# Kernel tuning notes

Hardware: AMD Instinct MI355X
Metric: run time of the kernel (lower is better)

Reference implementation:

```python
import jax, jax.numpy as jnp
import numpy as np

NUM_LAYERS = 4
HIDDEN = 64
IN_CH = 3
OUT_CH = 1


def setup_inputs() -> dict:
    key = jax.random.key(0)
    ks = jax.random.split(key, 16)
    s = 0.1  # weight init scale
    x = jax.random.normal(ks[0], (2, 64, 64, IN_CH), dtype=jnp.float32)
    lift_w = jax.random.normal(ks[1], (IN_CH, HIDDEN), dtype=jnp.float32) * s
    lift_b = jax.random.normal(ks[2], (HIDDEN,), dtype=jnp.float32) * s
    blk_w = jax.random.normal(ks[3], (NUM_LAYERS, HIDDEN, HIDDEN), dtype=jnp.float32) * s
    blk_b = jax.random.normal(ks[4], (NUM_LAYERS, HIDDEN), dtype=jnp.float32) * s
    q_w = jax.random.normal(ks[5], (NUM_LAYERS, HIDDEN, HIDDEN), dtype=jnp.float32) * s
    q_b = jax.random.normal(ks[6], (NUM_LAYERS, HIDDEN), dtype=jnp.float32) * s
    k_w = jax.random.normal(ks[7], (NUM_LAYERS, HIDDEN, HIDDEN), dtype=jnp.float32) * s
    k_b = jax.random.normal(ks[8], (NUM_LAYERS, HIDDEN), dtype=jnp.float32) * s
    v_w = jax.random.normal(ks[9], (NUM_LAYERS, HIDDEN, HIDDEN), dtype=jnp.float32) * s
    v_b = jax.random.normal(ks[10], (NUM_LAYERS, HIDDEN), dtype=jnp.float32) * s
    proj_w = jax.random.normal(ks[11], (HIDDEN, OUT_CH), dtype=jnp.float32) * s
    proj_b = jax.random.normal(ks[12], (OUT_CH,), dtype=jnp.float32) * s
    return {"x": x, "lift_w": lift_w, "lift_b": lift_b,
            "blk_w": blk_w, "blk_b": blk_b,
            "q_w": q_w, "q_b": q_b, "k_w": k_w, "k_b": k_b,
            "v_w": v_w, "v_b": v_b, "proj_w": proj_w, "proj_b": proj_b}


def reference(x, lift_w, lift_b, blk_w, blk_b, q_w, q_b, k_w, k_b, v_w, v_b, proj_w, proj_b):
    prefix = x.shape[:-1]           # (B, H, W)
    B = x.shape[0]
    xf = x.reshape(B, -1, x.shape[-1])   # [B, N, in_ch]
    N = xf.shape[1]
    h = xf @ lift_w + lift_b             # [B, N, d]
    d = h.shape[-1]
    scale = 1.0 / jnp.sqrt(jnp.float32(d))
    for i in range(NUM_LAYERS):
        q = h @ q_w[i] + q_b[i]
        k = h @ k_w[i] + k_b[i]
        v = h @ v_w[i] + v_b[i]
        # full dense kernel, as in torch.bmm(q, k^T)/sqrt(d)
        kern = jnp.einsum('bnd,bmd->bnm', q, k) * scale     # [B, N, N]
        integral = jnp.einsum('bnm,bmd->bnd', kern, v) / N  # [B, N, d]
        wh = h @ blk_w[i] + blk_b[i]
        h = jax.nn.gelu(wh + integral, approximate=False)   # torch F.gelu default = exact erf
    out = h @ proj_w + proj_b                               # [B, N, out_ch]
    return out.reshape(*prefix, out.shape[-1])
```

## Files before the change

### kernel.cpp

```cpp
#include <hip/hip_runtime.h>
#include <hip/hip_bf16.h>
#include <math.h>


#define NLAYER 4
#define NB 2
#define NN 4096
#define DD 64
#define RPB 32
#define NT 256
#define NBLK 256
#define SHP 68
#define C0F (1.0f/32768.0f)
#define PSZ 2304
#define NCH 128
#define CHW 18

typedef __hip_bfloat16 bf16;
typedef unsigned long long u64t;

__device__ __forceinline__ float b2f(const bf16 v) { return __bfloat162float(v); }

template <typename T> struct Acc;
template <> struct Acc<float> {
    static __device__ __forceinline__ float ld(const void* p, int i) { return ((const float*)p)[i]; }
    static __device__ __forceinline__ void st(void* p, int i, float v) { ((float*)p)[i] = v; }
};
template <> struct Acc<bf16> {
    static __device__ __forceinline__ float ld(const void* p, int i) { return b2f(((const bf16*)p)[i]); }
    static __device__ __forceinline__ void st(void* p, int i, float v) { ((bf16*)p)[i] = __float2bfloat16(v); }
};

__device__ __forceinline__ float gelu_exact(float x) {
    return 0.5f * x * (1.0f + erff(x * 0.70710678118654752f));
}

__device__ __forceinline__ float2 ldc2(const float* p) {
    u64t v = __hip_atomic_load((const u64t*)p, __ATOMIC_RELAXED, __HIP_MEMORY_SCOPE_AGENT);
    float2 r;
    r.x = __uint_as_float((unsigned)v);
    r.y = __uint_as_float((unsigned)(v >> 32));
    return r;
}
__device__ __forceinline__ void stc2(float* p, float a, float b) {
    u64t v = ((u64t)__float_as_uint(b) << 32) | (u64t)__float_as_uint(a);
    __hip_atomic_store((u64t*)p, v, __ATOMIC_RELAXED, __HIP_MEMORY_SCOPE_AGENT);
}
__device__ __forceinline__ unsigned ldw(unsigned* p) {
    return __hip_atomic_load(p, __ATOMIC_RELAXED, __HIP_MEMORY_SCOPE_AGENT);
}
__device__ __forceinline__ void stw(unsigned* p, unsigned v) {
    __hip_atomic_store(p, v, __ATOMIC_RELAXED, __HIP_MEMORY_SCOPE_AGENT);
}
__device__ __forceinline__ void pollw(unsigned* p, unsigned ep) {
    int guard = 0;
    while (ldw(p) < ep && ++guard < (1 << 17)) __builtin_amdgcn_s_sleep(8);
}

__device__ __forceinline__ void mm4x4(float (&acc)[4][4],
    float4 L0, float4 L1, float4 L2, float4 L3,
    float4 R0, float4 R1, float4 R2, float4 R3)
{
    const float L[4][4] = {{L0.x,L0.y,L0.z,L0.w},{L1.x,L1.y,L1.z,L1.w},
                           {L2.x,L2.y,L2.z,L2.w},{L3.x,L3.y,L3.z,L3.w}};
    const float R[4][4] = {{R0.x,R0.y,R0.z,R0.w},{R1.x,R1.y,R1.z,R1.w},
                           {R2.x,R2.y,R2.z,R2.w},{R3.x,R3.y,R3.z,R3.w}};
    #pragma unroll
    for (int a = 0; a < 4; a++)
        #pragma unroll
        for (int k = 0; k < 4; k++)
            #pragma unroll
            for (int b = 0; b < 4; b++)
                acc[a][b] += L[a][k] * R[k][b];
}

__device__ __forceinline__ void outer4x4(float (&acc)[4][4], float4 A, float4 B)
{
    const float Aa[4] = {A.x, A.y, A.z, A.w};
    const float Ba[4] = {B.x, B.y, B.z, B.w};
    #pragma unroll
    for (int a = 0; a < 4; a++)
        #pragma unroll
        for (int b = 0; b < 4; b++)
            acc[a][b] += Aa[a] * Ba[b];
}


template <typename T>
__device__ void run_net(
    const void* x, const void* lw, const void* lb,
    const void* blkw, const void* blkb,
    const void* qw, const void* qb, const void* kw, const void* kb,
    const void* vw, const void* vb, const void* pw, const void* pb,
    void* out, float* Gpart, float* Gg,
    unsigned* aflag, unsigned* cflag,
    float* smem, int blk, int t)
{
    float (*sH)[SHP] = (float(*)[SHP])(smem);
    float (*B1)[SHP] = (float(*)[SHP])(smem + 2176);
    float (*B2)[SHP] = (float(*)[SHP])(smem + 6528);
    float (*B3)[SHP] = (float(*)[SHP])(smem + 10880);
    float (*B4)[SHP] = (float(*)[SHP])(smem + 15232);
    float* PS  = smem + 10880;
    float* RED = smem + 10880;
    float* sS  = smem + 19584;
    float* suS = smem + 19648;
    float* bkS = smem + 19712;
    float* bqS = smem + 19776;
    float* bvS = smem + 19840;
    float* beS = smem + 19904;
    float (*red)[DD] = (float(*)[DD])(smem + 19968);

    const int row0 = blk * RPB;
    const int bb = blk >> 7;
    const int r = t >> 4, c4 = (t & 15) << 2;
    const int i4 = t >> 4, j4 = t & 15;
    const int r0 = i4 << 2, c0 = j4 << 2;

    #pragma unroll
    for (int a = 0; a < 2; a++) {
        const int row = r + 16 * a, gr = row0 + row;
        float x0 = Acc<T>::ld(x, gr * 3 + 0);
        float x1 = Acc<T>::ld(x, gr * 3 + 1);
        float x2 = Acc<T>::ld(x, gr * 3 + 2);
        float o[4];
        #pragma unroll
        for (int b = 0; b < 4; b++) {
            int c = c4 + b;
            o[b] = Acc<T>::ld(lb, c) + x0 * Acc<T>::ld(lw, c)
                 + x1 * Acc<T>::ld(lw, DD + c) + x2 * Acc<T>::ld(lw, 2 * DD + c);
        }
        *(float4*)&sH[row][c4] = make_float4(o[0], o[1], o[2], o[3]);
    }
    __syncthreads();

    for (int layer = 0; layer < NLAYER; layer++) {
        const unsigned ep = (unsigned)(layer + 1);
        float* GgL = Gg + (size_t)(layer * NB + bb) * PSZ;
        const int wOff = layer * DD * DD, bOff = layer * DD;

        {
            if (i4 <= j4) {
                float m[4][4];
                #pragma unroll
                for (int a = 0; a < 4; a++)
                    #pragma unroll
                    for (int b = 0; b < 4; b++) m[a][b] = 0.f;
                #pragma unroll 8
                for (int n = 0; n < RPB; n++)
                    outer4x4(m, *(const float4*)&sH[n][r0], *(const float4*)&sH[n][c0]);
                float* dst = PS + (i4 * (33 - i4) / 2 + (j4 - i4)) * 16;
                #pragma unroll
                for (int a = 0; a < 4; a++)
                    #pragma unroll
                    for (int b = 0; b < 4; b++) dst[a * 4 + b] = m[a][b];
            }
            if (t < DD) {
                float ss = 0.f;
                #pragma unroll 8
                for (int n = 0; n < RPB; n++) ss += sH[n][t];
                PS[2176 + t] = ss;
                PS[2240 + t] = 0.f;
            }
        }
        __syncthreads();
        {
            float* slot = Gpart + (size_t)blk * PSZ;
            #pragma unroll
            for (int k2 = 0; k2 < 4; k2++) {
                const int idx = 2 * (t + k2 * NT);
                stc2(&slot[idx], PS[idx], PS[idx + 1]);
            }
            if (t < 128) {
                const int idx = 2 * (t + 4 * NT);
                stc2(&slot[idx], PS[idx], PS[idx + 1]);
            }
        }
        __syncthreads();
        if (t == 0) stw(&aflag[blk], ep);

        for (int i2 = t; i2 < DD * DD; i2 += NT) {
            B2[i2 >> 6][i2 & 63] = Acc<T>::ld(vw, wOff + i2);
            B4[i2 >> 6][i2 & 63] = Acc<T>::ld(kw, wOff + i2);
        }
        if (t < DD) {
            bkS[t] = Acc<T>::ld(kb, bOff + t);
            bqS[t] = Acc<T>::ld(qb, bOff + t);
            bvS[t] = Acc<T>::ld(vb, bOff + t);
        }

        {
            if (t < NCH) pollw(&aflag[bb * NCH + t], ep);
            __syncthreads();
            const int chunk = blk & (NCH - 1);
            if (t < 144) {
                const int g = t / 9, p2 = t % 9;
                const float* base = Gpart + (size_t)(bb * NCH + g * 8) * PSZ
                                  + chunk * CHW + 2 * p2;
                float ax = 0.f, ay = 0.f;
                #pragma unroll
                for (int s2 = 0; s2 < 8; s2++) {
                    float2 v = ldc2(base + (size_t)s2 * PSZ);
                    ax += v.x; ay += v.y;
                }
                RED[g * 20 + 2 * p2]     = ax;
                RED[g * 20 + 2 * p2 + 1] = ay;
            }
            __syncthreads();
            if (t < 9) {
                float s0 = 0.f, s1 = 0.f;
                #pragma unroll
                for (int g = 0; g < 16; g++) {
                    s0 += RED[g * 20 + 2 * t];
                    s1 += RED[g * 20 + 2 * t + 1];
                }
                stc2(&GgL[chunk * CHW + 2 * t], s0, s1);
            }
            __syncthreads();
            if (t == 0) stw(&cflag[blk], ep);
        }

        {
            if (t < NCH) pollw(&cflag[bb * NCH + t], ep);
            __syncthreads();
            if (i4 <= j4) {
                const float* src = GgL + (i4 * (33 - i4) / 2 + (j4 - i4)) * 16;
                #pragma unroll
                for (int a = 0; a < 4; a++)
                    *(float4*)&B1[r0 + a][c0] = *(const float4*)&src[a * 4];
            } else {
                const float* src = GgL + (j4 * (33 - j4) / 2 + (i4 - j4)) * 16;
                #pragma unroll
                for (int a = 0; a < 4; a++)
                    #pragma unroll
                    for (int b = 0; b < 4; b++)
                        B1[r0 + a][c0 + b] = src[b * 4 + a];
            }
            if (t < DD) sS[t] = GgL[2176 + t];
            __syncthreads();
        }

        {
            float acc[4][4];
            #pragma unroll
            for (int a = 0; a < 4; a++)
                #pragma unroll
                for (int b = 0; b < 4; b++) acc[a][b] = sS[r0 + a] * bvS[c0 + b];
            #pragma unroll 2
            for (int e = 0; e < DD; e += 4)
                mm4x4(acc,
                      *(const float4*)&B1[r0 + 0][e], *(const float4*)&B1[r0 + 1][e],
                      *(const float4*)&B1[r0 + 2][e], *(const float4*)&B1[r0 + 3][e],
                      *(const float4*)&B2[e + 0][c0], *(const float4*)&B2[e + 1][c0],
                      *(const float4*)&B2[e + 2][c0], *(const float4*)&B2[e + 3][c0]);
            #pragma unroll
            for (int a = 0; a < 4; a++)
                *(float4*)&B3[r0 + a][c0] = make_float4(acc[a][0], acc[a][1], acc[a][2], acc[a][3]);
        }
        {
            const int c = t & 63, q = t >> 6;
            float u = 0.f;
            #pragma unroll
            for (int d2 = 0; d2 < 16; d2++) u += sS[q * 16 + d2] * B2[q * 16 + d2][c];
            red[q][c] = u;
        }
        __syncthreads();
        if (t < DD) suS[t] = red[0][t] + red[1][t] + red[2][t] + red[3][t] + (float)NN * bvS[t];
        __syncthreads();

        {
            float acc[4][4];
            #pragma unroll
            for (int a = 0; a < 4; a++)
                #pragma unroll
                for (int b = 0; b < 4; b++) acc[a][b] = bkS[r0 + a] * suS[c0 + b];
            #pragma unroll 4
            for (int d = 0; d < DD; d++)
                outer4x4(acc, *(const float4*)&B4[d][r0], *(const float4*)&B3[d][c0]);
            #pragma unroll
            for (int a = 0; a < 4; a++)
                *(float4*)&B2[r0 + a][c0] = make_float4(acc[a][0], acc[a][1], acc[a][2], acc[a][3]);
        }
        for (int i2 = t; i2 < DD * DD; i2 += NT) B1[i2 >> 6][i2 & 63] = Acc<T>::ld(qw, wOff + i2);
        __syncthreads();

        {
            float acc[4][4];
            #pragma unroll
            for (int a = 0; a < 4; a++)
                #pragma unroll
                for (int b = 0; b < 4; b++) acc[a][b] = 0.f;
            #pragma unroll 2
            for (int e = 0; e < DD; e += 4)
                mm4x4(acc,
                      *(const float4*)&B1[r0 + 0][e], *(const float4*)&B1[r0 + 1][e],
                      *(const float4*)&B1[r0 + 2][e], *(const float4*)&B1[r0 + 3][e],
                      *(const float4*)&B2[e + 0][c0], *(const float4*)&B2[e + 1][c0],
                      *(const float4*)&B2[e + 2][c0], *(const float4*)&B2[e + 3][c0]);
            #pragma unroll
            for (int a = 0; a < 4; a++) {
                float4 w;
                w.x = Acc<T>::ld(blkw, wOff + (r0 + a) * DD + c0 + 0) + C0F * acc[a][0];
                w.y = Acc<T>::ld(blkw, wOff + (r0 + a) * DD + c0 + 1) + C0F * acc[a][1];
                w.z = Acc<T>::ld(blkw, wOff + (r0 + a) * DD + c0 + 2) + C0F * acc[a][2];
                w.w = Acc<T>::ld(blkw, wOff + (r0 + a) * DD + c0 + 3) + C0F * acc[a][3];
                *(float4*)&B3[r0 + a][c0] = w;
            }
        }
        {
            const int c = t & 63, q = t >> 6;
            float u = 0.f;
            #pragma unroll
            for (int e2 = 0; e2 < 16; e2++) u += bqS[q * 16 + e2] * B2[q * 16 + e2][c];
            red[q][c] = u;
        }
        __syncthreads();
        if (t < DD) beS[t] = Acc<T>::ld(blkb, bOff + t)
                           + C0F * (red[0][t] + red[1][t] + red[2][t] + red[3][t]);
        __syncthreads();

        float o[2][4];
        #pragma unroll
        for (int a = 0; a < 2; a++) {
            const int row = r + 16 * a;
            float acc2[4];
            #pragma unroll
            for (int b = 0; b < 4; b++) acc2[b] = beS[c4 + b];
            for (int d = 0; d < DD; d++) {
                float hv = sH[row][d];
                float4 w4 = *(const float4*)&B3[d][c4];
                acc2[0] += hv * w4.x; acc2[1] += hv * w4.y;
                acc2[2] += hv * w4.z; acc2[3] += hv * w4.w;
            }
            #pragma unroll
            for (int b = 0; b < 4; b++) o[a][b] = gelu_exact(acc2[b]);
        }

        if (layer == NLAYER - 1) {
            float pbv = Acc<T>::ld(pb, 0);
            #pragma unroll
            for (int a = 0; a < 2; a++) {
                float p = 0.f;
                #pragma unroll
                for (int b = 0; b < 4; b++) p += o[a][b] * Acc<T>::ld(pw, c4 + b);
                p += __shfl_xor(p, 1);
                p += __shfl_xor(p, 2);
                p += __shfl_xor(p, 4);
                p += __shfl_xor(p, 8);
                if ((t & 15) == 0) Acc<T>::st(out, row0 + r + 16 * a, p + pbv);
            }
        } else {
            __syncthreads();
            #pragma unroll
            for (int a = 0; a < 2; a++)
                *(float4*)&sH[r + 16 * a][c4] =
                    make_float4(o[a][0], o[a][1], o[a][2], o[a][3]);
            __syncthreads();
        }
    }
}

__global__ __launch_bounds__(NT) void gno_kernel(
    const void* x, const void* lw, const void* lb,
    const void* blkw, const void* blkb,
    const void* qw, const void* qb, const void* kw, const void* kb,
    const void* vw, const void* vb, const void* pw, const void* pb,
    void* out, float* Gpart, float* Gg, unsigned* bar)
{
    __shared__ alignas(16) float smem[20224];
    __shared__ int stot;

    const int blk = blockIdx.x, t = threadIdx.x;

    if (t == 0) stot = 0;
    __syncthreads();
    int cdt = 0;
    const unsigned int* xw = (const unsigned int*)x;
    for (int i = t; i < 8192; i += NT) {
        unsigned u = xw[i] & 0xFFFFu;
        int e = (u >> 7) & 0xFF;
        cdt += (u == 0u || (e >= 100 && e <= 142)) ? 1 : 0;
    }
    atomicAdd(&stot, cdt);
    __syncthreads();
    const bool isbf = (stot > 4915);

    unsigned* aflag = bar;
    unsigned* cflag = bar + 256;

    if (isbf)
        run_net<bf16>(x, lw, lb, blkw, blkb, qw, qb, kw, kb, vw, vb, pw, pb,
                      out, Gpart, Gg, aflag, cflag, smem, blk, t);
    else
        run_net<float>(x, lw, lb, blkw, blkb, qw, qb, kw, kb, vw, vb, pw, pb,
                       out, Gpart, Gg, aflag, cflag, smem, blk, t);
}

extern "C" void kernel_launch(void* const* d_in, const int* in_sizes, int n_in,
                              void* d_out, int out_size, void* d_ws, size_t ws_size,
                              hipStream_t stream)
{
    const void* x    = d_in[0];
    const void* lw   = d_in[1];
    const void* lb   = d_in[2];
    const void* blkw = d_in[3];
    const void* blkb = d_in[4];
    const void* qw   = d_in[5];
    const void* qb   = d_in[6];
    const void* kw   = d_in[7];
    const void* kb   = d_in[8];
    const void* vw   = d_in[9];
    const void* vb   = d_in[10];
    const void* pw   = d_in[11];
    const void* pb   = d_in[12];

    unsigned* bar = (unsigned*)d_ws;
    float* Gpart  = (float*)d_ws + 512;
    float* Gg     = Gpart + (size_t)NBLK * PSZ;

    hipMemsetAsync(bar, 0, 512 * sizeof(unsigned), stream);
    gno_kernel<<<NBLK, NT, 0, stream>>>(x, lw, lb, blkw, blkb, qw, qb, kw, kb,
                                        vw, vb, pw, pb, d_out, Gpart, Gg, bar);
}
```

Measured before the change: 170.5 us.

## Precompute Wq·Wk^T before the Gram wait and detect dtype from input size on host

Moves the Q·K^T weight-product computation (plus the bias cross terms qk, kq and qbk) ahead of the cross-block Gram reduction wait, so it overlaps with polling. It also restructures the effective-weight composition to reuse that product and eliminate one 64x64 matmul stage. Separately, the host now picks bf16 or fp32 from the input byte size, which skips the per-block dtype-detection scan. The spin-wait sleep is shortened and its guard extended. In exchange, shared memory use grows and the kernel now depends on fixed input sizes to choose a mode.

```diff
diff --git a/kernel.cpp b/kernel.cpp
--- a/kernel.cpp
+++ b/kernel.cpp
@@ -54,7 +54,7 @@
 }
 __device__ __forceinline__ void pollw(unsigned* p, unsigned ep) {
     int guard = 0;
-    while (ldw(p) < ep && ++guard < (1 << 17)) __builtin_amdgcn_s_sleep(8);
+    while (ldw(p) < ep && ++guard < (1 << 18)) __builtin_amdgcn_s_sleep(2);
 }
 
 __device__ __forceinline__ void mm4x4(float (&acc)[4][4],
@@ -74,6 +74,23 @@
                 acc[a][b] += L[a][k] * R[k][b];
 }
 
+__device__ __forceinline__ void mmNT4x4(float (&acc)[4][4],
+    float4 L0, float4 L1, float4 L2, float4 L3,
+    float4 R0, float4 R1, float4 R2, float4 R3)
+{
+    const float L[4][4] = {{L0.x,L0.y,L0.z,L0.w},{L1.x,L1.y,L1.z,L1.w},
+                           {L2.x,L2.y,L2.z,L2.w},{L3.x,L3.y,L3.z,L3.w}};
+    const float R[4][4] = {{R0.x,R0.y,R0.z,R0.w},{R1.x,R1.y,R1.z,R1.w},
+                           {R2.x,R2.y,R2.z,R2.w},{R3.x,R3.y,R3.z,R3.w}};
+    #pragma unroll
+    for (int a = 0; a < 4; a++)
+        #pragma unroll
+        for (int b = 0; b < 4; b++)
+            #pragma unroll
+            for (int k = 0; k < 4; k++)
+                acc[a][b] += L[a][k] * R[b][k];
+}
+
 __device__ __forceinline__ void outer4x4(float (&acc)[4][4], float4 A, float4 B)
 {
     const float Aa[4] = {A.x, A.y, A.z, A.w};
@@ -85,6 +102,18 @@
             acc[a][b] += Aa[a] * Ba[b];
 }
 
+
+#define SM_SS   23936
+#define SM_SU   24000
+#define SM_BK   24064
+#define SM_BQ   24128
+#define SM_BV   24192
+#define SM_BE   24256
+#define SM_QK   24320
+#define SM_KQ   24384
+#define SM_QBK  24448
+#define SM_RED  24512
+#define SM_TOT  24768
 
 template <typename T>
 __device__ void run_net(
@@ -101,15 +130,19 @@
     float (*B2)[SHP] = (float(*)[SHP])(smem + 6528);
     float (*B3)[SHP] = (float(*)[SHP])(smem + 10880);
     float (*B4)[SHP] = (float(*)[SHP])(smem + 15232);
+    float (*B5)[SHP] = (float(*)[SHP])(smem + 19584);
     float* PS  = smem + 10880;
     float* RED = smem + 10880;
-    float* sS  = smem + 19584;
-    float* suS = smem + 19648;
-    float* bkS = smem + 19712;
-    float* bqS = smem + 19776;
-    float* bvS = smem + 19840;
-    float* beS = smem + 19904;
-    float (*red)[DD] = (float(*)[DD])(smem + 19968);
+    float* sS  = smem + SM_SS;
+    float* suS = smem + SM_SU;
+    float* bkS = smem + SM_BK;
+    float* bqS = smem + SM_BQ;
+    float* bvS = smem + SM_BV;
+    float* beS = smem + SM_BE;
+    float* qkS = smem + SM_QK;
+    float* kqS = smem + SM_KQ;
+    float* qbkS = smem + SM_QBK;
+    float (*red)[DD] = (float(*)[DD])(smem + SM_RED);
 
     const int row0 = blk * RPB;
     const int bb = blk >> 7;
@@ -180,7 +213,7 @@
         if (t == 0) stw(&aflag[blk], ep);
 
         for (int i2 = t; i2 < DD * DD; i2 += NT) {
-            B2[i2 >> 6][i2 & 63] = Acc<T>::ld(vw, wOff + i2);
+            B1[i2 >> 6][i2 & 63] = Acc<T>::ld(qw, wOff + i2);
             B4[i2 >> 6][i2 & 63] = Acc<T>::ld(kw, wOff + i2);
         }
         if (t < DD) {
@@ -221,20 +254,58 @@
         }
 
         {
+            float acc[4][4];
+            #pragma unroll
+            for (int a = 0; a < 4; a++)
+                #pragma unroll
+                for (int b = 0; b < 4; b++) acc[a][b] = 0.f;
+            #pragma unroll 2
+            for (int e = 0; e < DD; e += 4)
+                mmNT4x4(acc,
+                      *(const float4*)&B1[r0 + 0][e], *(const float4*)&B1[r0 + 1][e],
+                      *(const float4*)&B1[r0 + 2][e], *(const float4*)&B1[r0 + 3][e],
+                      *(const float4*)&B4[c0 + 0][e], *(const float4*)&B4[c0 + 1][e],
+                      *(const float4*)&B4[c0 + 2][e], *(const float4*)&B4[c0 + 3][e]);
+            #pragma unroll
+            for (int a = 0; a < 4; a++)
+                *(float4*)&B2[r0 + a][c0] = make_float4(acc[a][0], acc[a][1], acc[a][2], acc[a][3]);
+
+            if (t < DD) {
+                float u = 0.f;
+                for (int e = 0; e < DD; e++) u += B1[t][e] * bkS[e];
+                qkS[t] = u;
+            } else if (t < 2 * DD) {
+                const int rr = t - DD;
+                float u = 0.f;
+                for (int e = 0; e < DD; e++) u += B4[rr][e] * bqS[e];
+                kqS[rr] = u;
+            } else if (t == 2 * DD) {
+                float u = 0.f;
+                for (int e = 0; e < DD; e++) u += bqS[e] * bkS[e];
+                qbkS[0] = u;
+            }
+        }
+        __syncthreads();
+        for (int i2 = t; i2 < DD * DD; i2 += NT) {
+            B1[i2 >> 6][i2 & 63] = Acc<T>::ld(vw, wOff + i2);
+            B4[i2 >> 6][i2 & 63] = Acc<T>::ld(blkw, wOff + i2);
+        }
+
+        {
             if (t < NCH) pollw(&cflag[bb * NCH + t], ep);
             __syncthreads();
             if (i4 <= j4) {
                 const float* src = GgL + (i4 * (33 - i4) / 2 + (j4 - i4)) * 16;
                 #pragma unroll
                 for (int a = 0; a < 4; a++)
-                    *(float4*)&B1[r0 + a][c0] = *(const float4*)&src[a * 4];
+                    *(float4*)&B3[r0 + a][c0] = *(const float4*)&src[a * 4];
             } else {
                 const float* src = GgL + (j4 * (33 - j4) / 2 + (i4 - j4)) * 16;
                 #pragma unroll
                 for (int a = 0; a < 4; a++)
                     #pragma unroll
                     for (int b = 0; b < 4; b++)
-                        B1[r0 + a][c0 + b] = src[b * 4 + a];
+                        B3[r0 + a][c0 + b] = src[b * 4 + a];
             }
             if (t < DD) sS[t] = GgL[2176 + t];
             __syncthreads();
@@ -249,19 +320,19 @@
             #pragma unroll 2
             for (int e = 0; e < DD; e += 4)
                 mm4x4(acc,
-                      *(const float4*)&B1[r0 + 0][e], *(const float4*)&B1[r0 + 1][e],
-                      *(const float4*)&B1[r0 + 2][e], *(const float4*)&B1[r0 + 3][e],
-                      *(const float4*)&B2[e + 0][c0], *(const float4*)&B2[e + 1][c0],
-                      *(const float4*)&B2[e + 2][c0], *(const float4*)&B2[e + 3][c0]);
-            #pragma unroll
-            for (int a = 0; a < 4; a++)
-                *(float4*)&B3[r0 + a][c0] = make_float4(acc[a][0], acc[a][1], acc[a][2], acc[a][3]);
+                      *(const float4*)&B3[r0 + 0][e], *(const float4*)&B3[r0 + 1][e],
+                      *(const float4*)&B3[r0 + 2][e], *(const float4*)&B3[r0 + 3][e],
+                      *(const float4*)&B1[e + 0][c0], *(const float4*)&B1[e + 1][c0],
+                      *(const float4*)&B1[e + 2][c0], *(const float4*)&B1[e + 3][c0]);
+            #pragma unroll
+            for (int a = 0; a < 4; a++)
+                *(float4*)&B5[r0 + a][c0] = make_float4(acc[a][0], acc[a][1], acc[a][2], acc[a][3]);
         }
         {
             const int c = t & 63, q = t >> 6;
             float u = 0.f;
             #pragma unroll
-            for (int d2 = 0; d2 < 16; d2++) u += sS[q * 16 + d2] * B2[q * 16 + d2][c];
+            for (int d2 = 0; d2 < 16; d2++) u += sS[q * 16 + d2] * B1[q * 16 + d2][c];
             red[q][c] = u;
         }
         __syncthreads();
@@ -273,50 +344,35 @@
             #pragma unroll
             for (int a = 0; a < 4; a++)
                 #pragma unroll
-                for (int b = 0; b < 4; b++) acc[a][b] = bkS[r0 + a] * suS[c0 + b];
-            #pragma unroll 4
-            for (int d = 0; d < DD; d++)
-                outer4x4(acc, *(const float4*)&B4[d][r0], *(const float4*)&B3[d][c0]);
-            #pragma unroll
-            for (int a = 0; a < 4; a++)
-                *(float4*)&B2[r0 + a][c0] = make_float4(acc[a][0], acc[a][1], acc[a][2], acc[a][3]);
-        }
-        for (int i2 = t; i2 < DD * DD; i2 += NT) B1[i2 >> 6][i2 & 63] = Acc<T>::ld(qw, wOff + i2);
-        __syncthreads();
-
-        {
-            float acc[4][4];
-            #pragma unroll
-            for (int a = 0; a < 4; a++)
-                #pragma unroll
-                for (int b = 0; b < 4; b++) acc[a][b] = 0.f;
+                for (int b = 0; b < 4; b++) acc[a][b] = qkS[r0 + a] * suS[c0 + b];
             #pragma unroll 2
             for (int e = 0; e < DD; e += 4)
                 mm4x4(acc,
-                      *(const float4*)&B1[r0 + 0][e], *(const float4*)&B1[r0 + 1][e],
-                      *(const float4*)&B1[r0 + 2][e], *(const float4*)&B1[r0 + 3][e],
-                      *(const float4*)&B2[e + 0][c0], *(const float4*)&B2[e + 1][c0],
-                      *(const float4*)&B2[e + 2][c0], *(const float4*)&B2[e + 3][c0]);
-            #pragma unroll
-            for (int a = 0; a < 4; a++) {
-                float4 w;
-                w.x = Acc<T>::ld(blkw, wOff + (r0 + a) * DD + c0 + 0) + C0F * acc[a][0];
-                w.y = Acc<T>::ld(blkw, wOff + (r0 + a) * DD + c0 + 1) + C0F * acc[a][1];
-                w.z = Acc<T>::ld(blkw, wOff + (r0 + a) * DD + c0 + 2) + C0F * acc[a][2];
-                w.w = Acc<T>::ld(blkw, wOff + (r0 + a) * DD + c0 + 3) + C0F * acc[a][3];
-                *(float4*)&B3[r0 + a][c0] = w;
-            }
-        }
-        {
-            const int c = t & 63, q = t >> 6;
-            float u = 0.f;
-            #pragma unroll
-            for (int e2 = 0; e2 < 16; e2++) u += bqS[q * 16 + e2] * B2[q * 16 + e2][c];
-            red[q][c] = u;
-        }
-        __syncthreads();
-        if (t < DD) beS[t] = Acc<T>::ld(blkb, bOff + t)
-                           + C0F * (red[0][t] + red[1][t] + red[2][t] + red[3][t]);
+                      *(const float4*)&B2[r0 + 0][e], *(const float4*)&B2[r0 + 1][e],
+                      *(const float4*)&B2[r0 + 2][e], *(const float4*)&B2[r0 + 3][e],
+                      *(const float4*)&B5[e + 0][c0], *(const float4*)&B5[e + 1][c0],
+                      *(const float4*)&B5[e + 2][c0], *(const float4*)&B5[e + 3][c0]);
+            float wloc[4][4];
+            #pragma unroll
+            for (int a = 0; a < 4; a++)
+                #pragma unroll
+                for (int b = 0; b < 4; b++)
+                    wloc[a][b] = B4[r0 + a][c0 + b] + C0F * acc[a][b];
+            {
+                const int c = t & 63, q = t >> 6;
+                float u = 0.f;
+                #pragma unroll
+                for (int e2 = 0; e2 < 16; e2++) u += kqS[q * 16 + e2] * B5[q * 16 + e2][c];
+                red[q][c] = u;
+            }
+            __syncthreads();
+            #pragma unroll
+            for (int a = 0; a < 4; a++)
+                *(float4*)&B3[r0 + a][c0] = make_float4(wloc[a][0], wloc[a][1], wloc[a][2], wloc[a][3]);
+            if (t < DD) beS[t] = Acc<T>::ld(blkb, bOff + t)
+                               + C0F * (red[0][t] + red[1][t] + red[2][t] + red[3][t]
+                                        + qbkS[0] * suS[t]);
+        }
         __syncthreads();
 
         float o[2][4];
@@ -365,25 +421,30 @@
     const void* blkw, const void* blkb,
     const void* qw, const void* qb, const void* kw, const void* kb,
     const void* vw, const void* vb, const void* pw, const void* pb,
-    void* out, float* Gpart, float* Gg, unsigned* bar)
-{
-    __shared__ alignas(16) float smem[20224];
+    void* out, float* Gpart, float* Gg, unsigned* bar, int mode)
+{
+    __shared__ alignas(16) float smem[SM_TOT];
     __shared__ int stot;
 
     const int blk = blockIdx.x, t = threadIdx.x;
 
-    if (t == 0) stot = 0;
-    __syncthreads();
-    int cdt = 0;
-    const unsigned int* xw = (const unsigned int*)x;
-    for (int i = t; i < 8192; i += NT) {
-        unsigned u = xw[i] & 0xFFFFu;
-        int e = (u >> 7) & 0xFF;
-        cdt += (u == 0u || (e >= 100 && e <= 142)) ? 1 : 0;
+    bool isbf;
+    if (mode >= 0) {
+        isbf = (mode == 1);
+    } else {
+        if (t == 0) stot = 0;
+        __syncthreads();
+        int cdt = 0;
+        const unsigned int* xw = (const unsigned int*)x;
+        for (int i = t; i < 8192; i += NT) {
+            unsigned u = xw[i] & 0xFFFFu;
+            int e = (u >> 7) & 0xFF;
+            cdt += (u == 0u || (e >= 100 && e <= 142)) ? 1 : 0;
+        }
+        atomicAdd(&stot, cdt);
+        __syncthreads();
+        isbf = (stot > 4915);
     }
-    atomicAdd(&stot, cdt);
-    __syncthreads();
-    const bool isbf = (stot > 4915);
 
     unsigned* aflag = bar;
     unsigned* cflag = bar + 256;
@@ -414,11 +475,17 @@
     const void* pw   = d_in[11];
     const void* pb   = d_in[12];
 
+    int mode = -1;
+    if (in_sizes && n_in > 0) {
+        if (in_sizes[0] == 49152) mode = 1;
+        else if (in_sizes[0] == 98304) mode = 0;
+    }
+
     unsigned* bar = (unsigned*)d_ws;
     float* Gpart  = (float*)d_ws + 512;
     float* Gg     = Gpart + (size_t)NBLK * PSZ;
 
     hipMemsetAsync(bar, 0, 512 * sizeof(unsigned), stream);
     gno_kernel<<<NBLK, NT, 0, stream>>>(x, lw, lb, blkw, blkb, qw, qb, kw, kb,
-                                        vw, vb, pw, pb, d_out, Gpart, Gg, bar);
-}
+                                        vw, vb, pw, pb, d_out, Gpart, Gg, bar, mode);
+}
```

Result: faster. 159.4 us (-6.5%).

## Reassociate per-layer weight algebra to overlap row work with the global reduction

Applied to the files above, without the earlier changes.

Restructures the per-layer math so that h·Wq, the product of that with Wk transposed, and h·Wblk are computed per row block before waiting on the cross-block Gram reduction flag. Only the small Gram-dependent terms remain after the wait, which shortens the critical path after the barrier. The kernel also decides bf16 vs fp32 on the host from input byte sizes, skipping the in-kernel data-type sniffing pass. It also shortens the poll sleep and sets launch bounds to one block. In exchange it uses more shared memory and does extra per-row matmuls.

```diff
diff --git a/kernel.cpp b/kernel.cpp
--- a/kernel.cpp
+++ b/kernel.cpp
@@ -19,6 +19,27 @@
 typedef __hip_bfloat16 bf16;
 typedef unsigned long long u64t;
 
+#define O_SH   0
+#define O_HQ   2176
+#define O_HA   4352
+#define O_HWB  6528
+#define O_W1   8704
+#define O_W4   13056
+#define O_W5   17408
+#define O_B3   21760
+#define O_SS   26112
+#define O_SU   26176
+#define O_BK   26240
+#define O_BQ   26304
+#define O_BV   26368
+#define O_VR   26432
+#define O_KQ   26496
+#define O_HK   26560
+#define O_QBK  26624
+#define O_RED  26640
+#define O_RED2 26896
+#define SM_TOT 27152
+
 __device__ __forceinline__ float b2f(const bf16 v) { return __bfloat162float(v); }
 
 template <typename T> struct Acc;
@@ -54,7 +75,7 @@
 }
 __device__ __forceinline__ void pollw(unsigned* p, unsigned ep) {
     int guard = 0;
-    while (ldw(p) < ep && ++guard < (1 << 17)) __builtin_amdgcn_s_sleep(8);
+    while (ldw(p) < ep && ++guard < (1 << 18)) __builtin_amdgcn_s_sleep(2);
 }
 
 __device__ __forceinline__ void mm4x4(float (&acc)[4][4],
@@ -85,7 +106,6 @@
             acc[a][b] += Aa[a] * Ba[b];
 }
 
-
 template <typename T>
 __device__ void run_net(
     const void* x, const void* lw, const void* lb,
@@ -96,26 +116,34 @@
     unsigned* aflag, unsigned* cflag,
     float* smem, int blk, int t)
 {
-    float (*sH)[SHP] = (float(*)[SHP])(smem);
-    float (*B1)[SHP] = (float(*)[SHP])(smem + 2176);
-    float (*B2)[SHP] = (float(*)[SHP])(smem + 6528);
-    float (*B3)[SHP] = (float(*)[SHP])(smem + 10880);
-    float (*B4)[SHP] = (float(*)[SHP])(smem + 15232);
-    float* PS  = smem + 10880;
-    float* RED = smem + 10880;
-    float* sS  = smem + 19584;
-    float* suS = smem + 19648;
-    float* bkS = smem + 19712;
-    float* bqS = smem + 19776;
-    float* bvS = smem + 19840;
-    float* beS = smem + 19904;
-    float (*red)[DD] = (float(*)[DD])(smem + 19968);
+    float (*sH)[SHP]  = (float(*)[SHP])(smem + O_SH);
+    float (*HQ)[SHP]  = (float(*)[SHP])(smem + O_HQ);
+    float (*HA)[SHP]  = (float(*)[SHP])(smem + O_HA);
+    float (*HWB)[SHP] = (float(*)[SHP])(smem + O_HWB);
+    float (*W1)[SHP]  = (float(*)[SHP])(smem + O_W1);
+    float (*W4)[SHP]  = (float(*)[SHP])(smem + O_W4);
+    float (*W5r)[SHP] = (float(*)[SHP])(smem + O_W5);
+    float (*B3)[SHP]  = (float(*)[SHP])(smem + O_B3);
+    float* PS  = smem + O_B3;
+    float* RED = smem + O_B3;
+    float* sS  = smem + O_SS;
+    float* suS = smem + O_SU;
+    float* bkS = smem + O_BK;
+    float* bqS = smem + O_BQ;
+    float* bvS = smem + O_BV;
+    float* vrS = smem + O_VR;
+    float* kqS = smem + O_KQ;
+    float* hkS = smem + O_HK;
+    float* qbkS = smem + O_QBK;
+    float (*red)[DD]  = (float(*)[DD])(smem + O_RED);
+    float (*red2)[DD] = (float(*)[DD])(smem + O_RED2);
 
     const int row0 = blk * RPB;
     const int bb = blk >> 7;
     const int r = t >> 4, c4 = (t & 15) << 2;
     const int i4 = t >> 4, j4 = t & 15;
     const int r0 = i4 << 2, c0 = j4 << 2;
+    const int Ltr = t & 63, gtr = t >> 6;
 
     #pragma unroll
     for (int a = 0; a < 2; a++) {
@@ -180,8 +208,8 @@
         if (t == 0) stw(&aflag[blk], ep);
 
         for (int i2 = t; i2 < DD * DD; i2 += NT) {
-            B2[i2 >> 6][i2 & 63] = Acc<T>::ld(vw, wOff + i2);
-            B4[i2 >> 6][i2 & 63] = Acc<T>::ld(kw, wOff + i2);
+            W1[i2 >> 6][i2 & 63] = Acc<T>::ld(qw, wOff + i2);
+            W4[i2 >> 6][i2 & 63] = Acc<T>::ld(kw, wOff + i2);
         }
         if (t < DD) {
             bkS[t] = Acc<T>::ld(kb, bOff + t);
@@ -220,6 +248,70 @@
             if (t == 0) stw(&cflag[blk], ep);
         }
 
+        #pragma unroll
+        for (int k = 0; k < 16; k++) {
+            const int i = (Ltr + gtr + 4 * k) & 63;
+            W5r[i][Ltr] = W4[Ltr][i];
+        }
+        #pragma unroll
+        for (int a = 0; a < 2; a++) {
+            const int row = r + 16 * a;
+            float acc[4] = {0.f, 0.f, 0.f, 0.f};
+            for (int d = 0; d < DD; d++) {
+                const float hv = sH[row][d];
+                const float4 w4v = *(const float4*)&W1[d][c4];
+                acc[0] += hv * w4v.x; acc[1] += hv * w4v.y;
+                acc[2] += hv * w4v.z; acc[3] += hv * w4v.w;
+            }
+            *(float4*)&HQ[row][c4] = make_float4(acc[0], acc[1], acc[2], acc[3]);
+        }
+        if (t < DD) {
+            float u = 0.f;
+            for (int e = 0; e < DD; e++) u += W4[t][e] * bqS[e];
+            kqS[t] = u;
+        } else if (t == DD) {
+            float u = 0.f;
+            for (int e = 0; e < DD; e++) u += bqS[e] * bkS[e];
+            qbkS[0] = u;
+        }
+        __syncthreads();
+
+        #pragma unroll
+        for (int a = 0; a < 2; a++) {
+            const int row = r + 16 * a;
+            float acc[4] = {0.f, 0.f, 0.f, 0.f};
+            for (int d = 0; d < DD; d++) {
+                const float hv = HQ[row][d];
+                const float4 w4v = *(const float4*)&W5r[d][c4];
+                acc[0] += hv * w4v.x; acc[1] += hv * w4v.y;
+                acc[2] += hv * w4v.z; acc[3] += hv * w4v.w;
+            }
+            *(float4*)&HA[row][c4] = make_float4(acc[0], acc[1], acc[2], acc[3]);
+        }
+        if (t < RPB) {
+            float u = 0.f;
+            for (int e = 0; e < DD; e++) u += HQ[t][e] * bkS[e];
+            hkS[t] = u;
+        }
+        for (int i2 = t; i2 < DD * DD; i2 += NT) {
+            W1[i2 >> 6][i2 & 63] = Acc<T>::ld(vw, wOff + i2);
+            W4[i2 >> 6][i2 & 63] = Acc<T>::ld(blkw, wOff + i2);
+        }
+        __syncthreads();
+
+        #pragma unroll
+        for (int a = 0; a < 2; a++) {
+            const int row = r + 16 * a;
+            float acc[4] = {0.f, 0.f, 0.f, 0.f};
+            for (int d = 0; d < DD; d++) {
+                const float hv = sH[row][d];
+                const float4 w4v = *(const float4*)&W4[d][c4];
+                acc[0] += hv * w4v.x; acc[1] += hv * w4v.y;
+                acc[2] += hv * w4v.z; acc[3] += hv * w4v.w;
+            }
+            *(float4*)&HWB[row][c4] = make_float4(acc[0], acc[1], acc[2], acc[3]);
+        }
+
         {
             if (t < NCH) pollw(&cflag[bb * NCH + t], ep);
             __syncthreads();
@@ -227,14 +319,14 @@
                 const float* src = GgL + (i4 * (33 - i4) / 2 + (j4 - i4)) * 16;
                 #pragma unroll
                 for (int a = 0; a < 4; a++)
-                    *(float4*)&B1[r0 + a][c0] = *(const float4*)&src[a * 4];
+                    *(float4*)&B3[r0 + a][c0] = *(const float4*)&src[a * 4];
             } else {
                 const float* src = GgL + (j4 * (33 - j4) / 2 + (i4 - j4)) * 16;
                 #pragma unroll
                 for (int a = 0; a < 4; a++)
                     #pragma unroll
                     for (int b = 0; b < 4; b++)
-                        B1[r0 + a][c0 + b] = src[b * 4 + a];
+                        B3[r0 + a][c0 + b] = src[b * 4 + a];
             }
             if (t < DD) sS[t] = GgL[2176 + t];
             __syncthreads();
@@ -249,91 +341,54 @@
             #pragma unroll 2
             for (int e = 0; e < DD; e += 4)
                 mm4x4(acc,
-                      *(const float4*)&B1[r0 + 0][e], *(const float4*)&B1[r0 + 1][e],
-                      *(const float4*)&B1[r0 + 2][e], *(const float4*)&B1[r0 + 3][e],
-                      *(const float4*)&B2[e + 0][c0], *(const float4*)&B2[e + 1][c0],
-                      *(const float4*)&B2[e + 2][c0], *(const float4*)&B2[e + 3][c0]);
+                      *(const float4*)&B3[r0 + 0][e], *(const float4*)&B3[r0 + 1][e],
+                      *(const float4*)&B3[r0 + 2][e], *(const float4*)&B3[r0 + 3][e],
+                      *(const float4*)&W1[e + 0][c0], *(const float4*)&W1[e + 1][c0],
+                      *(const float4*)&W1[e + 2][c0], *(const float4*)&W1[e + 3][c0]);
             #pragma unroll
             for (int a = 0; a < 4; a++)
-                *(float4*)&B3[r0 + a][c0] = make_float4(acc[a][0], acc[a][1], acc[a][2], acc[a][3]);
+                *(float4*)&W5r[r0 + a][c0] = make_float4(acc[a][0], acc[a][1], acc[a][2], acc[a][3]);
         }
         {
             const int c = t & 63, q = t >> 6;
             float u = 0.f;
             #pragma unroll
-            for (int d2 = 0; d2 < 16; d2++) u += sS[q * 16 + d2] * B2[q * 16 + d2][c];
+            for (int d2 = 0; d2 < 16; d2++) u += sS[q * 16 + d2] * W1[q * 16 + d2][c];
             red[q][c] = u;
         }
         __syncthreads();
         if (t < DD) suS[t] = red[0][t] + red[1][t] + red[2][t] + red[3][t] + (float)NN * bvS[t];
-        __syncthreads();
-
-        {
-            float acc[4][4];
-            #pragma unroll
-            for (int a = 0; a < 4; a++)
-                #pragma unroll
-                for (int b = 0; b < 4; b++) acc[a][b] = bkS[r0 + a] * suS[c0 + b];
-            #pragma unroll 4
-            for (int d = 0; d < DD; d++)
-                outer4x4(acc, *(const float4*)&B4[d][r0], *(const float4*)&B3[d][c0]);
-            #pragma unroll
-            for (int a = 0; a < 4; a++)
-                *(float4*)&B2[r0 + a][c0] = make_float4(acc[a][0], acc[a][1], acc[a][2], acc[a][3]);
-        }
-        for (int i2 = t; i2 < DD * DD; i2 += NT) B1[i2 >> 6][i2 & 63] = Acc<T>::ld(qw, wOff + i2);
-        __syncthreads();
-
-        {
-            float acc[4][4];
-            #pragma unroll
-            for (int a = 0; a < 4; a++)
-                #pragma unroll
-                for (int b = 0; b < 4; b++) acc[a][b] = 0.f;
-            #pragma unroll 2
-            for (int e = 0; e < DD; e += 4)
-                mm4x4(acc,
-                      *(const float4*)&B1[r0 + 0][e], *(const float4*)&B1[r0 + 1][e],
-                      *(const float4*)&B1[r0 + 2][e], *(const float4*)&B1[r0 + 3][e],
-                      *(const float4*)&B2[e + 0][c0], *(const float4*)&B2[e + 1][c0],
-                      *(const float4*)&B2[e + 2][c0], *(const float4*)&B2[e + 3][c0]);
-            #pragma unroll
-            for (int a = 0; a < 4; a++) {
-                float4 w;
-                w.x = Acc<T>::ld(blkw, wOff + (r0 + a) * DD + c0 + 0) + C0F * acc[a][0];
-                w.y = Acc<T>::ld(blkw, wOff + (r0 + a) * DD + c0 + 1) + C0F * acc[a][1];
-                w.z = Acc<T>::ld(blkw, wOff + (r0 + a) * DD + c0 + 2) + C0F * acc[a][2];
-                w.w = Acc<T>::ld(blkw, wOff + (r0 + a) * DD + c0 + 3) + C0F * acc[a][3];
-                *(float4*)&B3[r0 + a][c0] = w;
-            }
-        }
         {
             const int c = t & 63, q = t >> 6;
             float u = 0.f;
             #pragma unroll
-            for (int e2 = 0; e2 < 16; e2++) u += bqS[q * 16 + e2] * B2[q * 16 + e2][c];
-            red[q][c] = u;
-        }
-        __syncthreads();
-        if (t < DD) beS[t] = Acc<T>::ld(blkb, bOff + t)
-                           + C0F * (red[0][t] + red[1][t] + red[2][t] + red[3][t]);
+            for (int e2 = 0; e2 < 16; e2++) u += kqS[q * 16 + e2] * W5r[q * 16 + e2][c];
+            red2[q][c] = u;
+        }
+        __syncthreads();
+        if (t < DD) vrS[t] = Acc<T>::ld(blkb, bOff + t)
+                           + C0F * (red2[0][t] + red2[1][t] + red2[2][t] + red2[3][t]
+                                    + qbkS[0] * suS[t]);
         __syncthreads();
 
         float o[2][4];
         #pragma unroll
         for (int a = 0; a < 2; a++) {
             const int row = r + 16 * a;
-            float acc2[4];
-            #pragma unroll
-            for (int b = 0; b < 4; b++) acc2[b] = beS[c4 + b];
+            float acc2[4] = {0.f, 0.f, 0.f, 0.f};
             for (int d = 0; d < DD; d++) {
-                float hv = sH[row][d];
-                float4 w4 = *(const float4*)&B3[d][c4];
-                acc2[0] += hv * w4.x; acc2[1] += hv * w4.y;
-                acc2[2] += hv * w4.z; acc2[3] += hv * w4.w;
-            }
-            #pragma unroll
-            for (int b = 0; b < 4; b++) o[a][b] = gelu_exact(acc2[b]);
+                const float hv = HA[row][d];
+                const float4 w4v = *(const float4*)&W5r[d][c4];
+                acc2[0] += hv * w4v.x; acc2[1] += hv * w4v.y;
+                acc2[2] += hv * w4v.z; acc2[3] += hv * w4v.w;
+            }
+            #pragma unroll
+            for (int b = 0; b < 4; b++) {
+                float val = HWB[row][c4 + b]
+                          + C0F * (acc2[b] + hkS[row] * suS[c4 + b])
+                          + vrS[c4 + b];
+                o[a][b] = gelu_exact(val);
+            }
         }
 
         if (layer == NLAYER - 1) {
@@ -350,7 +405,6 @@
                 if ((t & 15) == 0) Acc<T>::st(out, row0 + r + 16 * a, p + pbv);
             }
         } else {
-            __syncthreads();
             #pragma unroll
             for (int a = 0; a < 2; a++)
                 *(float4*)&sH[r + 16 * a][c4] =
@@ -360,30 +414,35 @@
     }
 }
 
-__global__ __launch_bounds__(NT) void gno_kernel(
+__global__ __launch_bounds__(NT, 1) void gno_kernel(
     const void* x, const void* lw, const void* lb,
     const void* blkw, const void* blkb,
     const void* qw, const void* qb, const void* kw, const void* kb,
     const void* vw, const void* vb, const void* pw, const void* pb,
-    void* out, float* Gpart, float* Gg, unsigned* bar)
+    void* out, float* Gpart, float* Gg, unsigned* bar, int mode)
 {
-    __shared__ alignas(16) float smem[20224];
+    __shared__ alignas(16) float smem[SM_TOT];
     __shared__ int stot;
 
     const int blk = blockIdx.x, t = threadIdx.x;
 
-    if (t == 0) stot = 0;
-    __syncthreads();
-    int cdt = 0;
-    const unsigned int* xw = (const unsigned int*)x;
-    for (int i = t; i < 8192; i += NT) {
-        unsigned u = xw[i] & 0xFFFFu;
-        int e = (u >> 7) & 0xFF;
-        cdt += (u == 0u || (e >= 100 && e <= 142)) ? 1 : 0;
+    bool isbf;
+    if (mode >= 0) {
+        isbf = (mode == 1);
+    } else {
+        if (t == 0) stot = 0;
+        __syncthreads();
+        int cdt = 0;
+        const unsigned int* xw = (const unsigned int*)x;
+        for (int i = t; i < 8192; i += NT) {
+            unsigned u = xw[i] & 0xFFFFu;
+            int e = (u >> 7) & 0xFF;
+            cdt += (u == 0u || (e >= 100 && e <= 142)) ? 1 : 0;
+        }
+        atomicAdd(&stot, cdt);
+        __syncthreads();
+        isbf = (stot > 4915);
     }
-    atomicAdd(&stot, cdt);
-    __syncthreads();
-    const bool isbf = (stot > 4915);
 
     unsigned* aflag = bar;
     unsigned* cflag = bar + 256;
@@ -414,11 +473,17 @@
     const void* pw   = d_in[11];
     const void* pb   = d_in[12];
 
+    int mode = -1;
+    if (in_sizes && n_in > 0) {
+        if (in_sizes[0] == 49152) mode = 1;
+        else if (in_sizes[0] == 98304) mode = 0;
+    }
+
     unsigned* bar = (unsigned*)d_ws;
     float* Gpart  = (float*)d_ws + 512;
     float* Gg     = Gpart + (size_t)NBLK * PSZ;
 
-    hipMemsetAsync(bar, 0, 512 * sizeof(unsigned), stream);
+    (void)hipMemsetAsync(bar, 0, 512 * sizeof(unsigned), stream);
     gno_kernel<<<NBLK, NT, 0, stream>>>(x, lw, lb, blkw, blkb, qw, qb, kw, kb,
-                                        vw, vb, pw, pb, d_out, Gpart, Gg, bar);
-}
+                                        vw, vb, pw, pb, d_out, Gpart, Gg, bar, mode);
+}
```

New measurement: 177.6 us. +4.2%, slower.
